# Optimization experiments

Hardware: AMD Instinct MI355X
Metric: run time of the kernel (lower is better)

## Reference

```python
import jax, jax.numpy as jnp
import numpy as np
from jax import lax

DN = ('NCDHW', 'OIDHW', 'NCDHW')  # dimension numbers matching torch Conv3d (cross-correlation)


def setup_inputs() -> dict:
    key = jax.random.key(0)
    k0, k1, k2, k3 = jax.random.split(key, 4)
    B, P, C = 32, 2048, 512
    x = jax.random.normal(k0, (B, P, C), dtype=jnp.float32)
    w1 = jax.random.normal(k1, (1, 1, 1, 1, 1), dtype=jnp.float32)
    w2 = jax.random.normal(k2, (1, 1, 2, 2, 2), dtype=jnp.float32)
    w3 = jax.random.normal(k3, (1, 1, 3, 3, 3), dtype=jnp.float32)
    return {"x": x, "w1": w1, "w2": w2, "w3": w3}


def reference(x, w1, w2, w3):
    B, P, C = x.shape
    t = P // 16
    # [B,P,C] -> [B,C,t,4,4]
    xv = jnp.transpose(x, (0, 2, 1)).reshape(B, C, t, 4, 4)
    # x_shift: [B,t,C,4,4] -> [B*t, C, 4, 4]
    x_shift = jnp.transpose(xv, (0, 2, 1, 3, 4)).reshape(B * t, C, 4, 4)
    # channel mean -> [B,1,t,4,4]
    xm = jnp.mean(xv, axis=1, keepdims=True)
    # ST_1: 1x1x1 conv, no pad
    p1 = lax.conv_general_dilated(xm, w1, (1, 1, 1), 'VALID', dimension_numbers=DN)
    # ST_2: pad (left=1 on t,h,w), then 2x2x2 valid conv -> same shape
    xp = jnp.pad(xm, ((0, 0), (0, 0), (1, 0), (1, 0), (1, 0)))
    p2 = lax.conv_general_dilated(xp, w2, (1, 1, 1), 'VALID', dimension_numbers=DN)
    # ST_3: 3x3x3 conv with padding 1 -> same shape
    p3 = lax.conv_general_dilated(xm, w3, (1, 1, 1), [(1, 1), (1, 1), (1, 1)], dimension_numbers=DN)
    g = p1 + p2 + p3  # [B,1,t,4,4]
    # transpose(2,1) -> [B,t,1,4,4] -> [B*t,1,4,4]
    g = jnp.transpose(g, (0, 2, 1, 3, 4)).reshape(B * t, 1, 4, 4)
    out = x_shift * jax.nn.sigmoid(g)  # broadcast over C
    # back to [B,P,C]
    out = out.reshape(B, t, C, 4, 4)
    out = jnp.transpose(out, (0, 2, 1, 3, 4)).reshape(B, C, P)
    return jnp.transpose(out, (0, 2, 1))
```

## Files before the change

### kernel.cpp

```cpp
#include <hip/hip_runtime.h>
#include <math.h>

#define BB 32
#define PP 2048
#define CC 512
#define TT 128
#define NCHUNK 64
#define NBLK (BB*NCHUNK)

__global__ __launch_bounds__(256, 4) void fused2_kernel(
        const float* __restrict__ x,
        const float* __restrict__ w1, const float* __restrict__ w2,
        const float* __restrict__ w3, float* __restrict__ out) {
    __shared__ float sm[4][16];
    __shared__ float sg[32];

    int bid = blockIdx.x;
    int wg  = ((bid & 7) << 8) | (bid >> 3);
    int b  = wg >> 6;
    int c  = wg & 63;
    int t0 = c << 1;

    int tid = threadIdx.x;
    int row = tid >> 4;
    int seg = tid & 15;

    const float4* xb = (const float4*)x + (size_t)b * (PP * CC / 4);
    const float4* xp0 = xb + (size_t)t0 * 2048;
    const float4* xp1 = xp0 + 2048;

    float4 v0[8], v1[8];
    #pragma unroll
    for (int k = 0; k < 8; ++k) v0[k] = xp0[row * 128 + seg + 16 * k];
    #pragma unroll
    for (int k = 0; k < 8; ++k) v1[k] = xp1[row * 128 + seg + 16 * k];

    int hr     = tid >> 3;
    int hu     = tid & 7;
    int hplane = hr >> 4;
    int hrow   = hr & 15;
    int ht     = hplane ? (t0 + 2) : (t0 - 1);
    bool hv    = (ht >= 0) && (ht < TT);
    float ha = 0.0f, hb2 = 0.0f;
    if (hv) {
        const float4* hp = xb + (size_t)ht * 2048 + hrow * 128;
        #pragma unroll
        for (int k = 0; k < 8; ++k) {
            float4 u = hp[hu + 8 * (2 * k)];
            float4 w = hp[hu + 8 * (2 * k + 1)];
            ha  += (u.x + u.y) + (u.z + u.w);
            hb2 += (w.x + w.y) + (w.z + w.w);
        }
    }
    float hs = ha + hb2;
    hs += __shfl_xor(hs, 1, 64);
    hs += __shfl_xor(hs, 2, 64);
    hs += __shfl_xor(hs, 4, 64);

    float s0 = 0.0f, s1 = 0.0f;
    #pragma unroll
    for (int k = 0; k < 8; ++k) s0 += (v0[k].x + v0[k].y) + (v0[k].z + v0[k].w);
    #pragma unroll
    for (int k = 0; k < 8; ++k) s1 += (v1[k].x + v1[k].y) + (v1[k].z + v1[k].w);
    #pragma unroll
    for (int m = 1; m <= 8; m <<= 1) {
        s0 += __shfl_xor(s0, m, 64);
        s1 += __shfl_xor(s1, m, 64);
    }

    if (seg == 0) {
        sm[1][row] = s0 * (1.0f / 512.0f);
        sm[2][row] = s1 * (1.0f / 512.0f);
    }
    if (hu == 0) sm[hplane ? 3 : 0][hrow] = hv ? hs * (1.0f / 512.0f) : 0.0f;
    __syncthreads();

    if (tid < 32) {
        int q  = tid >> 4;
        int r  = tid & 15;
        int h  = r >> 2;
        int w_ = r & 3;
        float g = 0.0f;
        #pragma unroll
        for (int i = 0; i < 3; ++i) {
            #pragma unroll
            for (int j = 0; j < 3; ++j) {
                int hh = h + j - 1;
                if (hh < 0 || hh > 3) continue;
                #pragma unroll
                for (int k = 0; k < 3; ++k) {
                    int ww = w_ + k - 1;
                    if (ww < 0 || ww > 3) continue;
                    float wt = w3[i * 9 + j * 3 + k];
                    if (i < 2 && j < 2 && k < 2) wt += w2[i * 4 + j * 2 + k];
                    if (i == 1 && j == 1 && k == 1) wt += w1[0];
                    g += wt * sm[q + i][hh * 4 + ww];
                }
            }
        }
        sg[tid] = 1.0f / (1.0f + __expf(-g));
    }
    __syncthreads();

    float g0 = sg[row];
    float g1 = sg[16 + row];
    float4* ob = (float4*)out + (size_t)b * (PP * CC / 4) + (size_t)t0 * 2048;
    #pragma unroll
    for (int k = 0; k < 8; ++k) {
        float4 o = v0[k];
        o.x *= g0; o.y *= g0; o.z *= g0; o.w *= g0;
        ob[row * 128 + seg + 16 * k] = o;
    }
    #pragma unroll
    for (int k = 0; k < 8; ++k) {
        float4 o = v1[k];
        o.x *= g1; o.y *= g1; o.z *= g1; o.w *= g1;
        ob[2048 + row * 128 + seg + 16 * k] = o;
    }
}

extern "C" void kernel_launch(void* const* d_in, const int* in_sizes, int n_in,
                              void* d_out, int out_size, void* d_ws, size_t ws_size,
                              hipStream_t stream) {
    const float* x  = (const float*)d_in[0];
    const float* w1 = (const float*)d_in[1];
    const float* w2 = (const float*)d_in[2];
    const float* w3 = (const float*)d_in[3];
    float* out = (float*)d_out;

    fused2_kernel<<<NBLK, 256, 0, stream>>>(x, w1, w2, w3, out);
}
```

Baseline: 245.2 us.

## Process four time planes per block to amortize halo plane reads

Each block now handles four consecutive time planes with 512 threads instead of two planes with 256, halving the number of blocks. The two halo planes needed for the 3x3x3 temporal stencil are now shared across four output planes, reducing redundant global reads of neighbouring planes. Reduction and gating logic are extended to 6 mean planes and 64 gate values, and an empty asm constraint pins loaded registers. Larger blocks reduce the number of blocks available for scheduling.

Measured after the change: 241.8 us. About the same (-1.4%).

```diff
diff --git a/kernel.cpp b/kernel.cpp
--- a/kernel.cpp
+++ b/kernel.cpp
@@ -5,77 +5,82 @@
 #define PP 2048
 #define CC 512
 #define TT 128
-#define NCHUNK 64
-#define NBLK (BB*NCHUNK)
+#define TC 4
+#define NBLK (BB*TT/TC)
+#define THR 512
 
-__global__ __launch_bounds__(256, 4) void fused2_kernel(
+__global__ __launch_bounds__(THR, 4) void fused4_kernel(
         const float* __restrict__ x,
         const float* __restrict__ w1, const float* __restrict__ w2,
         const float* __restrict__ w3, float* __restrict__ out) {
-    __shared__ float sm[4][16];
-    __shared__ float sg[32];
+    __shared__ float sm[6][16];
+    __shared__ float sgate[64];
 
     int bid = blockIdx.x;
-    int wg  = ((bid & 7) << 8) | (bid >> 3);
-    int b  = wg >> 6;
-    int c  = wg & 63;
-    int t0 = c << 1;
+    int wg  = ((bid & 7) << 7) | (bid >> 3);
+    int b   = wg >> 5;
+    int t0  = (wg & 31) << 2;
+    int plane0 = b * TT + t0;
 
     int tid = threadIdx.x;
-    int row = tid >> 4;
-    int seg = tid & 15;
+    int row = tid >> 3;
+    int seg = tid & 7;
 
     const float4* xb = (const float4*)x + (size_t)b * (PP * CC / 4);
-    const float4* xp0 = xb + (size_t)t0 * 2048;
-    const float4* xp1 = xp0 + 2048;
+    const float4* xr = (const float4*)x + (size_t)plane0 * 2048 + row * 128;
 
-    float4 v0[8], v1[8];
+    float4 v[16];
     #pragma unroll
-    for (int k = 0; k < 8; ++k) v0[k] = xp0[row * 128 + seg + 16 * k];
-    #pragma unroll
-    for (int k = 0; k < 8; ++k) v1[k] = xp1[row * 128 + seg + 16 * k];
+    for (int k = 0; k < 16; ++k) v[k] = xr[seg + 8 * k];
 
-    int hr     = tid >> 3;
-    int hu     = tid & 7;
-    int hplane = hr >> 4;
-    int hrow   = hr & 15;
-    int ht     = hplane ? (t0 + 2) : (t0 - 1);
+    int hr2    = tid >> 4;
+    int hseg   = tid & 15;
+    int hplane = hr2 >> 4;
+    int hrw    = hr2 & 15;
+    int ht     = hplane ? (t0 + TC) : (t0 - 1);
     bool hv    = (ht >= 0) && (ht < TT);
-    float ha = 0.0f, hb2 = 0.0f;
+    float hs = 0.0f;
     if (hv) {
-        const float4* hp = xb + (size_t)ht * 2048 + hrow * 128;
+        const float4* hp = xb + (size_t)ht * 2048 + hrw * 128;
+        float ha = 0.f, hb2 = 0.f;
         #pragma unroll
-        for (int k = 0; k < 8; ++k) {
-            float4 u = hp[hu + 8 * (2 * k)];
-            float4 w = hp[hu + 8 * (2 * k + 1)];
+        for (int k = 0; k < 4; ++k) {
+            float4 u = hp[hseg + 16 * (2 * k)];
+            float4 w = hp[hseg + 16 * (2 * k + 1)];
             ha  += (u.x + u.y) + (u.z + u.w);
             hb2 += (w.x + w.y) + (w.z + w.w);
         }
+        hs = ha + hb2;
     }
-    float hs = ha + hb2;
+
+    float a0 = 0.f, a1 = 0.f, a2 = 0.f, a3 = 0.f;
+    #pragma unroll
+    for (int k = 0; k < 4; ++k) {
+        a0 += (v[4*k+0].x + v[4*k+0].y) + (v[4*k+0].z + v[4*k+0].w);
+        a1 += (v[4*k+1].x + v[4*k+1].y) + (v[4*k+1].z + v[4*k+1].w);
+        a2 += (v[4*k+2].x + v[4*k+2].y) + (v[4*k+2].z + v[4*k+2].w);
+        a3 += (v[4*k+3].x + v[4*k+3].y) + (v[4*k+3].z + v[4*k+3].w);
+    }
+    float s = (a0 + a1) + (a2 + a3);
+
+    #pragma unroll
+    for (int k = 0; k < 16; ++k)
+        asm volatile("" : "+v"(v[k].x), "+v"(v[k].y), "+v"(v[k].z), "+v"(v[k].w));
+
+    s += __shfl_xor(s, 1, 64);
+    s += __shfl_xor(s, 2, 64);
+    s += __shfl_xor(s, 4, 64);
+
     hs += __shfl_xor(hs, 1, 64);
     hs += __shfl_xor(hs, 2, 64);
     hs += __shfl_xor(hs, 4, 64);
+    hs += __shfl_xor(hs, 8, 64);
 
-    float s0 = 0.0f, s1 = 0.0f;
-    #pragma unroll
-    for (int k = 0; k < 8; ++k) s0 += (v0[k].x + v0[k].y) + (v0[k].z + v0[k].w);
-    #pragma unroll
-    for (int k = 0; k < 8; ++k) s1 += (v1[k].x + v1[k].y) + (v1[k].z + v1[k].w);
-    #pragma unroll
-    for (int m = 1; m <= 8; m <<= 1) {
-        s0 += __shfl_xor(s0, m, 64);
-        s1 += __shfl_xor(s1, m, 64);
-    }
-
-    if (seg == 0) {
-        sm[1][row] = s0 * (1.0f / 512.0f);
-        sm[2][row] = s1 * (1.0f / 512.0f);
-    }
-    if (hu == 0) sm[hplane ? 3 : 0][hrow] = hv ? hs * (1.0f / 512.0f) : 0.0f;
+    if (seg == 0)  sm[1 + (row >> 4)][row & 15] = s * (1.0f / 512.0f);
+    if (hseg == 0) sm[hplane ? 5 : 0][hrw] = hv ? hs * (1.0f / 512.0f) : 0.0f;
     __syncthreads();
 
-    if (tid < 32) {
+    if (tid < 64) {
         int q  = tid >> 4;
         int r  = tid & 15;
         int h  = r >> 2;
@@ -98,24 +103,17 @@
                 }
             }
         }
-        sg[tid] = 1.0f / (1.0f + __expf(-g));
+        sgate[tid] = 1.0f / (1.0f + __expf(-g));
     }
     __syncthreads();
 
-    float g0 = sg[row];
-    float g1 = sg[16 + row];
-    float4* ob = (float4*)out + (size_t)b * (PP * CC / 4) + (size_t)t0 * 2048;
+    float g = sgate[row];
+    float4* op = (float4*)out + (size_t)plane0 * 2048 + row * 128;
     #pragma unroll
-    for (int k = 0; k < 8; ++k) {
-        float4 o = v0[k];
-        o.x *= g0; o.y *= g0; o.z *= g0; o.w *= g0;
-        ob[row * 128 + seg + 16 * k] = o;
-    }
-    #pragma unroll
-    for (int k = 0; k < 8; ++k) {
-        float4 o = v1[k];
-        o.x *= g1; o.y *= g1; o.z *= g1; o.w *= g1;
-        ob[2048 + row * 128 + seg + 16 * k] = o;
+    for (int k = 0; k < 16; ++k) {
+        float4 o = v[k];
+        o.x *= g; o.y *= g; o.z *= g; o.w *= g;
+        op[seg + 8 * k] = o;
     }
 }
 
@@ -128,5 +126,5 @@
     const float* w3 = (const float*)d_in[3];
     float* out = (float*)d_out;
 
-    fused2_kernel<<<NBLK, 256, 0, stream>>>(x, w1, w2, w3, out);
+    fused4_kernel<<<NBLK, THR, 0, stream>>>(x, w1, w2, w3, out);
 }
```
